# Kernel optimization log

Measured on AMD Instinct MI355X. Metric: run time of the kernel, lower is better.

The kernel has to match this reference:

```python
import jax, jax.numpy as jnp
import numpy as np

B, S, D = 8, 4096, 512
EPS = 1e-6


def setup_inputs() -> dict:
    key = jax.random.key(0)
    ks = jax.random.split(key, 9)
    scale = 1.0 / np.sqrt(D)
    inp = {
        "x_seq": jax.random.normal(ks[0], (B, S, D), dtype=jnp.float32),
        "Wq": jax.random.uniform(ks[1], (D, D), jnp.float32, -scale, scale),
        "bq": jax.random.uniform(ks[2], (D,), jnp.float32, -scale, scale),
        "Wk": jax.random.uniform(ks[3], (D, D), jnp.float32, -scale, scale),
        "bk": jax.random.uniform(ks[4], (D,), jnp.float32, -scale, scale),
        "Wv": jax.random.uniform(ks[5], (D, D), jnp.float32, -scale, scale),
        "bv": jax.random.uniform(ks[6], (D,), jnp.float32, -scale, scale),
        "Wa": jax.random.uniform(ks[7], (D, D), jnp.float32, -scale, scale),
        "ba": jax.random.uniform(ks[8], (D,), jnp.float32, -scale, scale),
    }
    return inp


def _forward(x_seq, Wq, bq, Wk, bk, Wv, bv, Wa, ba):
    # Precompute all projections for the whole sequence (big GEMMs).
    q = jax.nn.relu(jnp.einsum('bsd,ed->bse', x_seq, Wq) + bq)  # phi = relu
    k = jax.nn.relu(jnp.einsum('bsd,ed->bse', x_seq, Wk) + bk)
    v = jnp.einsum('bsd,ed->bse', x_seq, Wv) + bv
    a = jax.nn.sigmoid(jnp.einsum('bsd,ed->bse', x_seq, Wa) + ba)

    # time-major for scan: (S, B, D)
    qs, ks_, vs, as_ = (jnp.swapaxes(t, 0, 1) for t in (q, k, v, a))

    def step(carry, inp):
        s, z = carry                      # s: (B,D,D), z: (B,D)
        q_t, k_t, v_t, a_t = inp
        s = a_t[:, :, None] * s + k_t[:, :, None] * v_t[:, None, :]
        z = a_t * z + k_t
        num = jnp.einsum('bi,bij->bj', q_t, s)
        den = jnp.sum(q_t * z, axis=-1, keepdims=True) + EPS
        return (s, z), num / den

    s0 = jnp.zeros((x_seq.shape[0], x_seq.shape[2], x_seq.shape[2]), x_seq.dtype)
    z0 = jnp.zeros((x_seq.shape[0], x_seq.shape[2]), x_seq.dtype)
    _, ys = jax.lax.scan(step, (s0, z0), (qs, ks_, vs, as_))
    return jnp.swapaxes(ys, 0, 1)  # (B, S, D)


def reference(x_seq, Wq, bq, Wk, bk, Wv, bv, Wa, ba):
    return _forward(x_seq, Wq, bq, Wk, bk, Wv, bv, Wa, ba)
```

## Files before the change

kernel.cpp:

```cpp
#include <hip/hip_runtime.h>
#include <hip/hip_bf16.h>
#include <cstdint>
#include <cstddef>

#define D_DIM 512
#define B_DIM 8
#define S_DIM 4096
#define M_DIM (B_DIM * S_DIM)
#define CHUNK 64
#define NCHUNK (S_DIM / CHUNK)
#define NSEG 8
#define CSEG (NCHUNK / NSEG)
#define EPS_C 1e-6f

typedef __attribute__((ext_vector_type(8))) short bf16x8;
typedef __attribute__((ext_vector_type(4))) float f32x4;

#define GLOAD_LDS16(src, dst)                                              \
  __builtin_amdgcn_global_load_lds(                                        \
      (const __attribute__((address_space(1))) void*)(src),                \
      (__attribute__((address_space(3))) void*)(dst), 16, 0, 0)

__device__ __forceinline__ unsigned short f2bf(float f) {
  uint32_t u = __float_as_uint(f);
  u = (u + 0x7fffu + ((u >> 16) & 1u)) >> 16;
  return (unsigned short)u;
}
__device__ __forceinline__ float bf2f(unsigned short s) { return __uint_as_float(((uint32_t)s) << 16); }

__global__ void cvt_f32_bf16(const float* __restrict__ in, unsigned short* __restrict__ out, int n4) {
  int i = blockIdx.x * blockDim.x + threadIdx.x;
  int stride = gridDim.x * blockDim.x;
  for (; i < n4; i += stride) {
    float4 f = ((const float4*)in)[i];
    ushort4 o;
    o.x = f2bf(f.x); o.y = f2bf(f.y); o.z = f2bf(f.z); o.w = f2bf(f.w);
    ((ushort4*)out)[i] = o;
  }
}

#define TM 128
#define TN 128
#define BK 32

__global__ __launch_bounds__(256) void proj_gemm(
    const unsigned short* __restrict__ Xb,
    const unsigned short* __restrict__ Wb,
    const float* __restrict__ bq, const float* __restrict__ bk,
    const float* __restrict__ bv, const float* __restrict__ ba,
    unsigned short* __restrict__ q_ws, unsigned short* __restrict__ k_ws,
    unsigned short* __restrict__ v_ws, unsigned short* __restrict__ g_ws) {
  __shared__ unsigned short SB[TM * BK + TN * BK];
  unsigned short* As = SB;
  unsigned short* Bs = SB + TM * BK;

  const int proj = blockIdx.z;
  const unsigned short* W = Wb + (size_t)proj * D_DIM * D_DIM;
  const int m0 = blockIdx.x * TM;
  const int n0 = blockIdx.y * TN;
  const int tid = threadIdx.x;
  const int lane = tid & 63;
  const int wave = tid >> 6;
  const int wm = (wave & 1) * 64;
  const int wn = (wave >> 1) * 64;
  const int quad = lane >> 4;
  const int l16 = lane & 15;

  f32x4 acc[4][4];
#pragma unroll
  for (int i = 0; i < 4; ++i)
#pragma unroll
    for (int j = 0; j < 4; ++j) acc[i][j] = (f32x4){0.f, 0.f, 0.f, 0.f};

  const int rw = lane >> 2;
  const int kq = (lane & 3) * 8;

  for (int kc = 0; kc < D_DIM; kc += BK) {
    __syncthreads();
    {
      const unsigned short* gA0 = &Xb[(size_t)(m0 + wave * 16 + rw) * D_DIM + kc + kq];
      const unsigned short* gA1 = &Xb[(size_t)(m0 + 64 + wave * 16 + rw) * D_DIM + kc + kq];
      const unsigned short* gB0 = &W[(size_t)(n0 + wave * 16 + rw) * D_DIM + kc + kq];
      const unsigned short* gB1 = &W[(size_t)(n0 + 64 + wave * 16 + rw) * D_DIM + kc + kq];
      GLOAD_LDS16(gA0, &As[(wave * 16) * BK]);
      GLOAD_LDS16(gA1, &As[(64 + wave * 16) * BK]);
      GLOAD_LDS16(gB0, &Bs[(wave * 16) * BK]);
      GLOAD_LDS16(gB1, &Bs[(64 + wave * 16) * BK]);
    }
    __syncthreads();

    bf16x8 afr[4], bfr[4];
#pragma unroll
    for (int im = 0; im < 4; ++im)
      afr[im] = *(const bf16x8*)&As[(wm + im * 16 + l16) * BK + quad * 8];
#pragma unroll
    for (int in = 0; in < 4; ++in)
      bfr[in] = *(const bf16x8*)&Bs[(wn + in * 16 + l16) * BK + quad * 8];
#pragma unroll
    for (int im = 0; im < 4; ++im)
#pragma unroll
      for (int in = 0; in < 4; ++in)
        acc[im][in] = __builtin_amdgcn_mfma_f32_16x16x32_bf16(afr[im], bfr[in], acc[im][in], 0, 0, 0);
  }

  __syncthreads();

  const float* bias = (proj == 0) ? bq : (proj == 1) ? bk : (proj == 2) ? bv : ba;
  unsigned short* outp = (proj == 0) ? q_ws : (proj == 1) ? k_ws : (proj == 2) ? v_ws : g_ws;
  const bool do_relu = (proj <= 1);
  unsigned short* EP = &SB[wave * 64 * 32];

#pragma unroll
  for (int p = 0; p < 2; ++p) {
#pragma unroll
    for (int half = 0; half < 2; ++half) {
      const int in = 2 * p + half;
      const int nn = n0 + wn + in * 16 + l16;
      const float bn = bias[nn];
#pragma unroll
      for (int im = 0; im < 4; ++im) {
#pragma unroll
        for (int vv = 0; vv < 4; ++vv) {
          float val = acc[im][in][vv] + bn;
          if (do_relu) val = fmaxf(val, 0.f);
          EP[(im * 16 + quad * 4 + vv) * 32 + half * 16 + l16] = f2bf(val);
        }
      }
    }
#pragma unroll
    for (int it = 0; it < 4; ++it) {
      const int row = it * 16 + (lane >> 2);
      const int ccol = (lane & 3) * 8;
      bf16x8 vdat = *(const bf16x8*)&EP[row * 32 + ccol];
      size_t gidx = (size_t)(m0 + wm + row) * D_DIM + (size_t)(n0 + wn + p * 32 + ccol);
      *(bf16x8*)&outp[gidx] = vdat;
    }
  }
}

__global__ __launch_bounds__(512) void prep(
    const unsigned short* __restrict__ q, const unsigned short* __restrict__ k,
    const unsigned short* __restrict__ g,
    unsigned short* __restrict__ qt, unsigned short* __restrict__ kt,
    unsigned short* __restrict__ kh,
    float* __restrict__ Af, float* __restrict__ khs) {
  __shared__ float segp[8][512];
  const int c = blockIdx.x, b = blockIdx.y;
  const int seg = threadIdx.x >> 6;
  const int t = threadIdx.x & 63;
  const int i0 = t * 8;
  const int r0 = seg * 8;
  const size_t t0 = (size_t)b * S_DIM + (size_t)c * CHUNK;
  const size_t cb = ((size_t)b * NCHUNK + c) * D_DIM;

  float sp[8];
#pragma unroll
  for (int j = 0; j < 8; ++j) sp[j] = 1.f;
  for (int r = 0; r < 8; ++r) {
    bf16x8 gv = *(const bf16x8*)&g[(t0 + r0 + r) * D_DIM + i0];
#pragma unroll
    for (int j = 0; j < 8; ++j)
      sp[j] *= 1.f / (1.f + __expf(-bf2f((unsigned short)gv[j])));
  }
  *(float4*)&segp[seg][i0] = *(float4*)&sp[0];
  *(float4*)&segp[seg][i0 + 4] = *(float4*)&sp[4];
  __syncthreads();

  float pre[8], tot[8];
#pragma unroll
  for (int j = 0; j < 8; ++j) { pre[j] = 1.f; tot[j] = 1.f; }
  for (int s2 = 0; s2 < 8; ++s2) {
    float4 v0 = *(const float4*)&segp[s2][i0];
    float4 v1 = *(const float4*)&segp[s2][i0 + 4];
    float v[8] = {v0.x, v0.y, v0.z, v0.w, v1.x, v1.y, v1.z, v1.w};
#pragma unroll
    for (int j = 0; j < 8; ++j) {
      tot[j] *= v[j];
      if (s2 < seg) pre[j] *= v[j];
    }
  }
  if (seg == 0) {
    float4 a0 = {tot[0], tot[1], tot[2], tot[3]};
    float4 a1 = {tot[4], tot[5], tot[6], tot[7]};
    *(float4*)&Af[cb + i0] = a0;
    *(float4*)&Af[cb + i0 + 4] = a1;
  }

  float cum[8], ssum[8];
#pragma unroll
  for (int j = 0; j < 8; ++j) { cum[j] = pre[j]; ssum[j] = 0.f; }
  for (int r = 0; r < 8; ++r) {
    size_t idx = (t0 + r0 + r) * D_DIM + i0;
    bf16x8 gv = *(const bf16x8*)&g[idx];
    bf16x8 qv8 = *(const bf16x8*)&q[idx];
    bf16x8 kv8 = *(const bf16x8*)&k[idx];
    bf16x8 oq, ok, okh;
#pragma unroll
    for (int j = 0; j < 8; ++j) {
      cum[j] *= 1.f / (1.f + __expf(-bf2f((unsigned short)gv[j])));
      float qv = bf2f((unsigned short)qv8[j]);
      float kv = bf2f((unsigned short)kv8[j]);
      oq[j] = (short)f2bf(qv * cum[j]);
      float inv = 1.f / cum[j];
      ok[j] = (short)f2bf(kv * inv);
      float khf = kv * (tot[j] * inv);
      okh[j] = (short)f2bf(khf);
      ssum[j] += khf;
    }
    *(bf16x8*)&qt[idx] = oq;
    *(bf16x8*)&kt[idx] = ok;
    *(bf16x8*)&kh[idx] = okh;
  }

  __syncthreads();
  *(float4*)&segp[seg][i0] = *(float4*)&ssum[0];
  *(float4*)&segp[seg][i0 + 4] = *(float4*)&ssum[4];
  __syncthreads();
  if (seg == 0) {
    float s[8];
#pragma unroll
    for (int j = 0; j < 8; ++j) s[j] = 0.f;
    for (int s2 = 0; s2 < 8; ++s2) {
      float4 v0 = *(const float4*)&segp[s2][i0];
      float4 v1 = *(const float4*)&segp[s2][i0 + 4];
      s[0] += v0.x; s[1] += v0.y; s[2] += v0.z; s[3] += v0.w;
      s[4] += v1.x; s[5] += v1.y; s[6] += v1.z; s[7] += v1.w;
    }
    float4 a0 = {s[0], s[1], s[2], s[3]};
    float4 a1 = {s[4], s[5], s[6], s[7]};
    *(float4*)&khs[cb + i0] = a0;
    *(float4*)&khs[cb + i0 + 4] = a1;
  }
}

__global__ __launch_bounds__(256) void transpose_cd(
    const unsigned short* __restrict__ in, unsigned short* __restrict__ outT) {
  __shared__ unsigned short tile[CHUNK][264];
  const int c = blockIdx.x, b = blockIdx.y;
  const size_t base_in = ((size_t)b * S_DIM + (size_t)c * CHUNK) * D_DIM;
  const size_t base_out = ((size_t)b * NCHUNK + c) * (size_t)D_DIM * CHUNK;
  const int tid = threadIdx.x;
#pragma unroll
  for (int h = 0; h < 2; ++h) {
    if (h) __syncthreads();
#pragma unroll
    for (int it = 0; it < 8; ++it) {
      int flat = (it * 256 + tid) * 8;
      int row = flat >> 8;
      int col = flat & 255;
      *(uint4*)&tile[row][col] = *(const uint4*)&in[base_in + (size_t)row * D_DIM + h * 256 + col];
    }
    __syncthreads();
#pragma unroll
    for (int it = 0; it < 8; ++it) {
      int wq = it * 256 + tid;
      int i_loc = wq >> 3;
      int r0 = (wq & 7) * 8;
      ushort4 v0, v1;
      v0.x = tile[r0 + 0][i_loc]; v0.y = tile[r0 + 1][i_loc];
      v0.z = tile[r0 + 2][i_loc]; v0.w = tile[r0 + 3][i_loc];
      v1.x = tile[r0 + 4][i_loc]; v1.y = tile[r0 + 5][i_loc];
      v1.z = tile[r0 + 6][i_loc]; v1.w = tile[r0 + 7][i_loc];
      size_t o = base_out + (size_t)(h * 256 + i_loc) * CHUNK + r0;
      *(ushort4*)&outT[o] = v0;
      *(ushort4*)&outT[o + 4] = v1;
    }
  }
}

__global__ __launch_bounds__(256) void intra(
    const unsigned short* __restrict__ qt, const unsigned short* kt,
    const unsigned short* __restrict__ VT,
    unsigned short* numI, float* __restrict__ rs) {
  __shared__ unsigned short P_lds[CHUNK][CHUNK + 8];
  const int c = blockIdx.x, b = blockIdx.y;
  const size_t t0 = (size_t)b * S_DIM + (size_t)c * CHUNK;
  const int lane = threadIdx.x & 63, w = threadIdx.x >> 6;
  const int l16 = lane & 15, q4 = lane >> 4;

  f32x4 accP[4];
#pragma unroll
  for (int n = 0; n < 4; ++n) accP[n] = (f32x4){0.f, 0.f, 0.f, 0.f};
#pragma unroll
  for (int ks = 0; ks < 16; ++ks) {
    bf16x8 afr = *(const bf16x8*)&qt[(t0 + 16 * w + l16) * D_DIM + 32 * ks + 8 * q4];
#pragma unroll
    for (int n = 0; n < 4; ++n) {
      bf16x8 bfr = *(const bf16x8*)&kt[(t0 + 16 * n + l16) * D_DIM + 32 * ks + 8 * q4];
      accP[n] = __builtin_amdgcn_mfma_f32_16x16x32_bf16(afr, bfr, accP[n], 0, 0, 0);
    }
  }
  float rsum[4] = {0.f, 0.f, 0.f, 0.f};
#pragma unroll
  for (int n = 0; n < 4; ++n) {
    int m = 16 * n + l16;
#pragma unroll
    for (int vv = 0; vv < 4; ++vv) {
      int r = 16 * w + 4 * q4 + vv;
      float pv = (m <= r) ? accP[n][vv] : 0.f;
      rsum[vv] += pv;
      P_lds[r][m] = f2bf(pv);
    }
  }
#pragma unroll
  for (int msk = 1; msk < 16; msk <<= 1) {
#pragma unroll
    for (int vv = 0; vv < 4; ++vv) rsum[vv] += __shfl_xor(rsum[vv], msk, 64);
  }
  if (l16 == 0) {
#pragma unroll
    for (int vv = 0; vv < 4; ++vv) rs[t0 + 16 * w + 4 * q4 + vv] = rsum[vv];
  }
  __syncthreads();
  bf16x8 pa0 = *(const bf16x8*)&P_lds[16 * w + l16][8 * q4];
  bf16x8 pa1 = *(const bf16x8*)&P_lds[16 * w + l16][32 + 8 * q4];
  const size_t vtb = ((size_t)b * NCHUNK + c) * (size_t)D_DIM * CHUNK;
#pragma unroll 4
  for (int nt = 0; nt < 32; ++nt) {
    bf16x8 b0 = *(const bf16x8*)&VT[vtb + (size_t)(nt * 16 + l16) * CHUNK + 8 * q4];
    bf16x8 b1 = *(const bf16x8*)&VT[vtb + (size_t)(nt * 16 + l16) * CHUNK + 32 + 8 * q4];
    f32x4 acc = (f32x4){0.f, 0.f, 0.f, 0.f};
    acc = __builtin_amdgcn_mfma_f32_16x16x32_bf16(pa0, b0, acc, 0, 0, 0);
    acc = __builtin_amdgcn_mfma_f32_16x16x32_bf16(pa1, b1, acc, 0, 0, 0);
#pragma unroll
    for (int vv = 0; vv < 4; ++vv)
      numI[(t0 + 16 * w + 4 * q4 + vv) * D_DIM + nt * 16 + l16] = f2bf(acc[vv]);
  }
}

__global__ __launch_bounds__(512) void zscan(
    const float* __restrict__ Af, const float* __restrict__ khs,
    float* __restrict__ zall, float* __restrict__ Pseg) {
  const int b = blockIdx.x;
  const int i = threadIdx.x;
  float z = 0.f, rp = 1.f;
  for (int c = 0; c < NCHUNK; ++c) {
    const size_t cb = ((size_t)b * NCHUNK + c) * D_DIM;
    zall[cb + i] = z;
    float af = Af[cb + i];
    z = fmaf(af, z, khs[cb + i]);
    rp *= af;
    if ((c & (CSEG - 1)) == CSEG - 1) {
      Pseg[((size_t)b * NSEG + (c / CSEG)) * D_DIM + i] = rp;
      rp = 1.f;
    }
  }
}

__global__ __launch_bounds__(512) void denk(
    const unsigned short* __restrict__ qt, const float* __restrict__ zall,
    float* rs_invden) {
  const int c = blockIdx.x, b = blockIdx.y;
  const int lane = threadIdx.x & 63, w = threadIdx.x >> 6;
  const size_t t0 = (size_t)b * S_DIM + (size_t)c * CHUNK;
  const size_t zb = ((size_t)b * NCHUNK + c) * D_DIM;
  float4 z0 = *(const float4*)&zall[zb + lane * 8];
  float4 z1 = *(const float4*)&zall[zb + lane * 8 + 4];
#pragma unroll
  for (int rr = 0; rr < 8; ++rr) {
    int r = 8 * w + rr;
    bf16x8 qv = *(const bf16x8*)&qt[(t0 + r) * D_DIM + lane * 8];
    float p = 0.f;
    p = fmaf(bf2f((unsigned short)qv[0]), z0.x, p);
    p = fmaf(bf2f((unsigned short)qv[1]), z0.y, p);
    p = fmaf(bf2f((unsigned short)qv[2]), z0.z, p);
    p = fmaf(bf2f((unsigned short)qv[3]), z0.w, p);
    p = fmaf(bf2f((unsigned short)qv[4]), z1.x, p);
    p = fmaf(bf2f((unsigned short)qv[5]), z1.y, p);
    p = fmaf(bf2f((unsigned short)qv[6]), z1.z, p);
    p = fmaf(bf2f((unsigned short)qv[7]), z1.w, p);
#pragma unroll
    for (int msk = 1; msk < 64; msk <<= 1) p += __shfl_xor(p, msk, 64);
    if (lane == 0) {
      float* iv = &rs_invden[t0 + r];
      *iv = 1.f / (p + *iv + EPS_C);
    }
  }
}

__global__ __launch_bounds__(512, 2) void useg_k(
    const unsigned short* __restrict__ khT, const unsigned short* __restrict__ VT,
    const float* __restrict__ Af, unsigned short* __restrict__ U) {
  __shared__ unsigned short VTl[2][128 * 64];
  const int s = blockIdx.x, jt = blockIdx.y, b = blockIdx.z;
  const int lane = threadIdx.x & 63, w = threadIdx.x >> 6;
  const int l16 = lane & 15, q4 = lane >> 4;
  const int j0 = jt * 128;
  const int iw = 64 * w;
  const int vrow = lane >> 3;
  const int vswz = (lane & 7) ^ (vrow & 7);

  f32x4 acc[4][8];
#pragma unroll
  for (int T = 0; T < 4; ++T)
#pragma unroll
    for (int h = 0; h < 8; ++h) acc[T][h] = (f32x4){0.f, 0.f, 0.f, 0.f};

  const size_t cb0 = ((size_t)b * NCHUNK + s * CSEG) * D_DIM;
  {
    const size_t ob0 = cb0 * CHUNK;
#pragma unroll
    for (int kk = 0; kk < 2; ++kk) {
      const int k = 2 * w + kk;
      GLOAD_LDS16(&VT[ob0 + (size_t)(j0 + 8 * k + vrow) * CHUNK + vswz * 8],
                  &VTl[0][k * 512]);
    }
  }
  bf16x8 a0[4], a1[4];
  {
    const size_t ob0 = cb0 * CHUNK;
#pragma unroll
    for (int T = 0; T < 4; ++T) {
      a0[T] = *(const bf16x8*)&khT[ob0 + (size_t)(iw + 16 * T + l16) * CHUNK + 8 * q4];
      a1[T] = *(const bf16x8*)&khT[ob0 + (size_t)(iw + 16 * T + l16) * CHUNK + 32 + 8 * q4];
    }
  }

  for (int cc = 0; cc < CSEG; ++cc) {
    const size_t cb = cb0 + (size_t)cc * D_DIM;
    __syncthreads();
    if (cc + 1 < CSEG) {
      const size_t obn = (cb + D_DIM) * CHUNK;
#pragma unroll
      for (int kk = 0; kk < 2; ++kk) {
        const int k = 2 * w + kk;
        GLOAD_LDS16(&VT[obn + (size_t)(j0 + 8 * k + vrow) * CHUNK + vswz * 8],
                    &VTl[(cc + 1) & 1][k * 512]);
      }
    }
#pragma unroll
    for (int T = 0; T < 4; ++T) {
      float4 af = *(const float4*)&Af[cb + iw + 16 * T + 4 * q4];
#pragma unroll
      for (int h = 0; h < 8; ++h) {
        acc[T][h][0] *= af.x; acc[T][h][1] *= af.y; acc[T][h][2] *= af.z; acc[T][h][3] *= af.w;
      }
    }
    const unsigned short* Vb = VTl[cc & 1];
#pragma unroll
    for (int h = 0; h < 8; ++h) {
      const int jpos = 16 * h + l16;
      const int swz = jpos & 7;
      bf16x8 bv0 = *(const bf16x8*)&Vb[jpos * 64 + ((q4 ^ swz) * 8)];
      bf16x8 bv1 = *(const bf16x8*)&Vb[jpos * 64 + (((4 + q4) ^ swz) * 8)];
#pragma unroll
      for (int T = 0; T < 4; ++T) {
        acc[T][h] = __builtin_amdgcn_mfma_f32_16x16x32_bf16(a0[T], bv0, acc[T][h], 0, 0, 0);
        acc[T][h] = __builtin_amdgcn_mfma_f32_16x16x32_bf16(a1[T], bv1, acc[T][h], 0, 0, 0);
      }
    }
    if (cc + 1 < CSEG) {
      const size_t obn = (cb + D_DIM) * CHUNK;
#pragma unroll
      for (int T = 0; T < 4; ++T) {
        a0[T] = *(const bf16x8*)&khT[obn + (size_t)(iw + 16 * T + l16) * CHUNK + 8 * q4];
        a1[T] = *(const bf16x8*)&khT[obn + (size_t)(iw + 16 * T + l16) * CHUNK + 32 + 8 * q4];
      }
    }
  }
  const size_t ub = ((size_t)b * NSEG + s) * D_DIM;
#pragma unroll
  for (int T = 0; T < 4; ++T)
#pragma unroll
    for (int h = 0; h < 8; ++h) {
      uint2 pk;
      pk.x = (uint32_t)f2bf(acc[T][h][0]) | ((uint32_t)f2bf(acc[T][h][1]) << 16);
      pk.y = (uint32_t)f2bf(acc[T][h][2]) | ((uint32_t)f2bf(acc[T][h][3]) << 16);
      *(uint2*)&U[(ub + j0 + 16 * h + l16) * (size_t)D_DIM + iw + 16 * T + 4 * q4] = pk;
    }
}

__global__ __launch_bounds__(256) void sscan(
    const float* __restrict__ Pseg, unsigned short* __restrict__ U) {
  const int b = blockIdx.y;
  const int flat = blockIdx.x * 256 + threadIdx.x;
  const int j = flat >> 6;
  const int i0 = (flat & 63) * 8;
  float acc[8];
#pragma unroll
  for (int t = 0; t < 8; ++t) acc[t] = 0.f;
  for (int s = 0; s < NSEG; ++s) {
    const size_t pb = ((size_t)b * NSEG + s) * D_DIM;
    unsigned short* up = &U[(pb + j) * (size_t)D_DIM + i0];
    uint4 u = *(const uint4*)up;
    float4 p0 = *(const float4*)&Pseg[pb + i0];
    float4 p1 = *(const float4*)&Pseg[pb + i0 + 4];
    float uv[8];
    uv[0] = bf2f((unsigned short)(u.x & 0xffff)); uv[1] = bf2f((unsigned short)(u.x >> 16));
    uv[2] = bf2f((unsigned short)(u.y & 0xffff)); uv[3] = bf2f((unsigned short)(u.y >> 16));
    uv[4] = bf2f((unsigned short)(u.z & 0xffff)); uv[5] = bf2f((unsigned short)(u.z >> 16));
    uv[6] = bf2f((unsigned short)(u.w & 0xffff)); uv[7] = bf2f((unsigned short)(u.w >> 16));
    uint4 o;
    o.x = (uint32_t)f2bf(acc[0]) | ((uint32_t)f2bf(acc[1]) << 16);
    o.y = (uint32_t)f2bf(acc[2]) | ((uint32_t)f2bf(acc[3]) << 16);
    o.z = (uint32_t)f2bf(acc[4]) | ((uint32_t)f2bf(acc[5]) << 16);
    o.w = (uint32_t)f2bf(acc[6]) | ((uint32_t)f2bf(acc[7]) << 16);
    *(uint4*)up = o;
    acc[0] = fmaf(p0.x, acc[0], uv[0]);
    acc[1] = fmaf(p0.y, acc[1], uv[1]);
    acc[2] = fmaf(p0.z, acc[2], uv[2]);
    acc[3] = fmaf(p0.w, acc[3], uv[3]);
    acc[4] = fmaf(p1.x, acc[4], uv[4]);
    acc[5] = fmaf(p1.y, acc[5], uv[5]);
    acc[6] = fmaf(p1.z, acc[6], uv[6]);
    acc[7] = fmaf(p1.w, acc[7], uv[7]);
  }
}

__global__ __launch_bounds__(512, 2) void scan2(
    const unsigned short* __restrict__ qt, const unsigned short* __restrict__ khT,
    const unsigned short* __restrict__ VT, const float* __restrict__ Af,
    const unsigned short* __restrict__ Sin,
    const unsigned short* __restrict__ numI, const float* __restrict__ invden,
    float* __restrict__ out) {
  __shared__ unsigned short STj[128][520];
  __shared__ unsigned short VTl[128 * 64];
  const int s = blockIdx.x, jt = blockIdx.y, b = blockIdx.z;
  const int lane = threadIdx.x & 63, w = threadIdx.x >> 6;
  const int l16 = lane & 15, q4 = lane >> 4;
  const int j0 = jt * 128;
  const int iw = 64 * w;
  const int rw = 16 * (w & 3);
  const int jo = 64 * (w >> 2);
  const int vrow = lane >> 3;
  const int vswz = (lane & 7) ^ (vrow & 7);

  f32x4 acc[4][8];

  {
    const size_t pb = ((size_t)b * NSEG + s) * D_DIM;
#pragma unroll
    for (int T = 0; T < 4; ++T)
#pragma unroll
      for (int h = 0; h < 8; ++h) {
        uint2 uu = *(const uint2*)&Sin[(pb + j0 + 16 * h + l16) * (size_t)D_DIM + iw + 16 * T + 4 * q4];
        acc[T][h][0] = bf2f((unsigned short)(uu.x & 0xffff));
        acc[T][h][1] = bf2f((unsigned short)(uu.x >> 16));
        acc[T][h][2] = bf2f((unsigned short)(uu.y & 0xffff));
        acc[T][h][3] = bf2f((unsigned short)(uu.y >> 16));
      }
  }

  for (int cc = 0; cc < CSEG; ++cc) {
    const int c = s * CSEG + cc;
    const size_t cb = ((size_t)b * NCHUNK + c) * D_DIM;
    const size_t t0 = (size_t)b * S_DIM + (size_t)c * CHUNK;
    const size_t ob = cb * CHUNK;
    const bool upd = (cc != CSEG - 1);

    bf16x8 a0[4], a1[4];
    if (upd) {
#pragma unroll
      for (int kk = 0; kk < 2; ++kk) {
        const int k = 2 * w + kk;
        GLOAD_LDS16(&VT[ob + (size_t)(j0 + 8 * k + vrow) * CHUNK + vswz * 8],
                    &VTl[k * 512]);
      }
#pragma unroll
      for (int T = 0; T < 4; ++T) {
        a0[T] = *(const bf16x8*)&khT[ob + (size_t)(iw + 16 * T + l16) * CHUNK + 8 * q4];
        a1[T] = *(const bf16x8*)&khT[ob + (size_t)(iw + 16 * T + l16) * CHUNK + 32 + 8 * q4];
      }
    }

#pragma unroll
    for (int T = 0; T < 4; ++T)
#pragma unroll
      for (int h = 0; h < 8; ++h) {
        uint2 pk;
        pk.x = (uint32_t)f2bf(acc[T][h][0]) | ((uint32_t)f2bf(acc[T][h][1]) << 16);
        pk.y = (uint32_t)f2bf(acc[T][h][2]) | ((uint32_t)f2bf(acc[T][h][3]) << 16);
        *(uint2*)&STj[16 * h + l16][iw + 16 * T + 4 * q4] = pk;
      }
    __syncthreads();

    {
      f32x4 accO[4];
#pragma unroll
      for (int h = 0; h < 4; ++h) accO[h] = (f32x4){0.f, 0.f, 0.f, 0.f};
#pragma unroll
      for (int ks = 0; ks < 16; ++ks) {
        bf16x8 afr = *(const bf16x8*)&qt[(t0 + rw + l16) * D_DIM + 32 * ks + 8 * q4];
#pragma unroll
        for (int h = 0; h < 4; ++h) {
          bf16x8 bfr = *(const bf16x8*)&STj[jo + 16 * h + l16][32 * ks + 8 * q4];
          accO[h] = __builtin_amdgcn_mfma_f32_16x16x32_bf16(afr, bfr, accO[h], 0, 0, 0);
        }
      }
#pragma unroll
      for (int h = 0; h < 4; ++h)
#pragma unroll
        for (int vv = 0; vv < 4; ++vv) {
          size_t t = t0 + rw + 4 * q4 + vv;
          int j = j0 + jo + 16 * h + l16;
          float idv = invden[t];
          float nI = bf2f(numI[t * D_DIM + j]);
          out[t * D_DIM + j] = (accO[h][vv] + nI) * idv;
        }
    }

    if (upd) {
#pragma unroll
      for (int T = 0; T < 4; ++T) {
        float4 af = *(const float4*)&Af[cb + iw + 16 * T + 4 * q4];
#pragma unroll
        for (int h = 0; h < 8; ++h) {
          acc[T][h][0] *= af.x; acc[T][h][1] *= af.y; acc[T][h][2] *= af.z; acc[T][h][3] *= af.w;
        }
      }
#pragma unroll
      for (int h = 0; h < 8; ++h) {
        const int jpos = 16 * h + l16;
        const int swz = jpos & 7;
        bf16x8 bv0 = *(const bf16x8*)&VTl[jpos * 64 + ((q4 ^ swz) * 8)];
        bf16x8 bv1 = *(const bf16x8*)&VTl[jpos * 64 + (((4 + q4) ^ swz) * 8)];
#pragma unroll
        for (int T = 0; T < 4; ++T) {
          acc[T][h] = __builtin_amdgcn_mfma_f32_16x16x32_bf16(a0[T], bv0, acc[T][h], 0, 0, 0);
          acc[T][h] = __builtin_amdgcn_mfma_f32_16x16x32_bf16(a1[T], bv1, acc[T][h], 0, 0, 0);
        }
      }
    }
    __syncthreads();
  }
}

extern "C" void kernel_launch(void* const* d_in, const int* in_sizes, int n_in,
                              void* d_out, int out_size, void* d_ws, size_t ws_size,
                              hipStream_t stream) {
  const float* x  = (const float*)d_in[0];
  const float* Wq = (const float*)d_in[1];
  const float* bq = (const float*)d_in[2];
  const float* Wk = (const float*)d_in[3];
  const float* bk = (const float*)d_in[4];
  const float* Wv = (const float*)d_in[5];
  const float* bv = (const float*)d_in[6];
  const float* Wa = (const float*)d_in[7];
  const float* ba = (const float*)d_in[8];
  float* out = (float*)d_out;

  const size_t MD2 = (size_t)M_DIM * D_DIM * 2;
  uint8_t* w = (uint8_t*)d_ws;
  unsigned short* xb   = (unsigned short*)w; w += MD2;
  unsigned short* wb   = (unsigned short*)w; w += (size_t)4 * D_DIM * D_DIM * 2;
  unsigned short* q_ws = (unsigned short*)w; w += MD2;
  unsigned short* k_ws = (unsigned short*)w; w += MD2;
  unsigned short* v_ws = (unsigned short*)w; w += MD2;
  unsigned short* g_ws = (unsigned short*)w; w += MD2;
  float* Af     = (float*)w; w += (size_t)B_DIM * NCHUNK * D_DIM * 4;
  float* khs    = (float*)w; w += (size_t)B_DIM * NCHUNK * D_DIM * 4;
  float* invden = (float*)w; w += (size_t)M_DIM * 4;

  unsigned short* qt   = xb;
  unsigned short* kt   = q_ws;
  unsigned short* kh   = k_ws;
  unsigned short* VT   = g_ws;
  unsigned short* khT  = v_ws;
  unsigned short* numI = q_ws;
  unsigned short* U    = k_ws;
  float* zall = (float*)wb;
  float* Pseg = (float*)((uint8_t*)wb + (1 << 20));

  cvt_f32_bf16<<<1024, 256, 0, stream>>>(x, xb, M_DIM * D_DIM / 4);
  cvt_f32_bf16<<<128, 256, 0, stream>>>(Wq, wb + 0 * D_DIM * D_DIM, D_DIM * D_DIM / 4);
  cvt_f32_bf16<<<128, 256, 0, stream>>>(Wk, wb + 1 * D_DIM * D_DIM, D_DIM * D_DIM / 4);
  cvt_f32_bf16<<<128, 256, 0, stream>>>(Wv, wb + 2 * D_DIM * D_DIM, D_DIM * D_DIM / 4);
  cvt_f32_bf16<<<128, 256, 0, stream>>>(Wa, wb + 3 * D_DIM * D_DIM, D_DIM * D_DIM / 4);

  proj_gemm<<<dim3(M_DIM / TM, D_DIM / TN, 4), 256, 0, stream>>>(
      xb, wb, bq, bk, bv, ba, q_ws, k_ws, v_ws, g_ws);

  prep<<<dim3(NCHUNK, B_DIM), 512, 0, stream>>>(q_ws, k_ws, g_ws, qt, kt, kh, Af, khs);
  transpose_cd<<<dim3(NCHUNK, B_DIM), 256, 0, stream>>>(v_ws, VT);
  transpose_cd<<<dim3(NCHUNK, B_DIM), 256, 0, stream>>>(kh, khT);
  zscan<<<B_DIM, 512, 0, stream>>>(Af, khs, zall, Pseg);
  intra<<<dim3(NCHUNK, B_DIM), 256, 0, stream>>>(qt, kt, VT, numI, invden);
  denk<<<dim3(NCHUNK, B_DIM), 512, 0, stream>>>(qt, zall, invden);
  useg_k<<<dim3(NSEG, 4, B_DIM), 512, 0, stream>>>(khT, VT, Af, U);
  sscan<<<dim3(128, B_DIM), 256, 0, stream>>>(Pseg, U);
  scan2<<<dim3(NSEG, 4, B_DIM), 512, 0, stream>>>(qt, khT, VT, Af, U, numI, invden, out);
}
```

Measured before the change: 505.8 us.

## Enlarge projection GEMM tiles with double-buffered swizzled LDS staging

Result: no change. 508.3 us (+0.5%).

```diff
diff --git a/kernel.cpp b/kernel.cpp
--- a/kernel.cpp
+++ b/kernel.cpp
@@ -39,96 +39,103 @@
   }
 }
 
-#define TM 128
-#define TN 128
-#define BK 32
-
-__global__ __launch_bounds__(256) void proj_gemm(
+#define PTM 256
+#define PTN 256
+#define PBK 64
+
+__global__ __launch_bounds__(512, 2) void proj_gemm(
     const unsigned short* __restrict__ Xb,
     const unsigned short* __restrict__ Wb,
     const float* __restrict__ bq, const float* __restrict__ bk,
     const float* __restrict__ bv, const float* __restrict__ ba,
     unsigned short* __restrict__ q_ws, unsigned short* __restrict__ k_ws,
     unsigned short* __restrict__ v_ws, unsigned short* __restrict__ g_ws) {
-  __shared__ unsigned short SB[TM * BK + TN * BK];
-  unsigned short* As = SB;
-  unsigned short* Bs = SB + TM * BK;
+  __shared__ unsigned short SB[2 * (PTM + PTN) * PBK];
 
   const int proj = blockIdx.z;
   const unsigned short* W = Wb + (size_t)proj * D_DIM * D_DIM;
-  const int m0 = blockIdx.x * TM;
-  const int n0 = blockIdx.y * TN;
-  const int tid = threadIdx.x;
-  const int lane = tid & 63;
-  const int wave = tid >> 6;
-  const int wm = (wave & 1) * 64;
-  const int wn = (wave >> 1) * 64;
-  const int quad = lane >> 4;
-  const int l16 = lane & 15;
-
-  f32x4 acc[4][4];
-#pragma unroll
-  for (int i = 0; i < 4; ++i)
-#pragma unroll
-    for (int j = 0; j < 4; ++j) acc[i][j] = (f32x4){0.f, 0.f, 0.f, 0.f};
-
-  const int rw = lane >> 2;
-  const int kq = (lane & 3) * 8;
-
-  for (int kc = 0; kc < D_DIM; kc += BK) {
+  const int m0 = blockIdx.x * PTM;
+  const int n0 = blockIdx.y * PTN;
+  const int lane = threadIdx.x & 63;
+  const int w = threadIdx.x >> 6;
+  const int l16 = lane & 15, q4 = lane >> 4;
+  const int wm = (w >> 2) * 128;
+  const int wn = (w & 3) * 64;
+
+  f32x4 acc[8][4];
+#pragma unroll
+  for (int m = 0; m < 8; ++m)
+#pragma unroll
+    for (int n = 0; n < 4; ++n) acc[m][n] = (f32x4){0.f, 0.f, 0.f, 0.f};
+
+  const int srow = lane >> 3;
+  const int sg = lane & 7;
+
+  auto STAGE = [&](int buf, int kc) {
+    unsigned short* A = SB + buf * ((PTM + PTN) * PBK);
+    unsigned short* Bs = A + PTM * PBK;
+#pragma unroll
+    for (int q = 0; q < 4; ++q) {
+      const int row = w * 32 + q * 8 + srow;
+      const int g = sg ^ (row & 7);
+      GLOAD_LDS16(&Xb[(size_t)(m0 + row) * D_DIM + kc + g * 8], &A[(w * 32 + q * 8) * PBK]);
+      GLOAD_LDS16(&W[(size_t)(n0 + row) * D_DIM + kc + g * 8], &Bs[(w * 32 + q * 8) * PBK]);
+    }
+  };
+
+  STAGE(0, 0);
+  __syncthreads();
+
+  for (int t = 0; t < D_DIM / PBK; ++t) {
+    const int cur = t & 1;
+    if (t + 1 < D_DIM / PBK) STAGE(cur ^ 1, (t + 1) * PBK);
+
+    const unsigned short* A = SB + cur * ((PTM + PTN) * PBK);
+    const unsigned short* Bs = A + PTM * PBK;
+    const int rsw = l16 & 7;
+#pragma unroll
+    for (int ks = 0; ks < 2; ++ks) {
+      const int gphys = ((ks * 4 + q4) ^ rsw) * 8;
+      bf16x8 afr[8], bfr[4];
+#pragma unroll
+      for (int m = 0; m < 8; ++m)
+        afr[m] = *(const bf16x8*)&A[(wm + m * 16 + l16) * PBK + gphys];
+#pragma unroll
+      for (int n = 0; n < 4; ++n)
+        bfr[n] = *(const bf16x8*)&Bs[(wn + n * 16 + l16) * PBK + gphys];
+#pragma unroll
+      for (int m = 0; m < 8; ++m)
+#pragma unroll
+        for (int n = 0; n < 4; ++n)
+          acc[m][n] = __builtin_amdgcn_mfma_f32_16x16x32_bf16(afr[m], bfr[n], acc[m][n], 0, 0, 0);
+    }
     __syncthreads();
-    {
-      const unsigned short* gA0 = &Xb[(size_t)(m0 + wave * 16 + rw) * D_DIM + kc + kq];
-      const unsigned short* gA1 = &Xb[(size_t)(m0 + 64 + wave * 16 + rw) * D_DIM + kc + kq];
-      const unsigned short* gB0 = &W[(size_t)(n0 + wave * 16 + rw) * D_DIM + kc + kq];
-      const unsigned short* gB1 = &W[(size_t)(n0 + 64 + wave * 16 + rw) * D_DIM + kc + kq];
-      GLOAD_LDS16(gA0, &As[(wave * 16) * BK]);
-      GLOAD_LDS16(gA1, &As[(64 + wave * 16) * BK]);
-      GLOAD_LDS16(gB0, &Bs[(wave * 16) * BK]);
-      GLOAD_LDS16(gB1, &Bs[(64 + wave * 16) * BK]);
-    }
-    __syncthreads();
-
-    bf16x8 afr[4], bfr[4];
-#pragma unroll
-    for (int im = 0; im < 4; ++im)
-      afr[im] = *(const bf16x8*)&As[(wm + im * 16 + l16) * BK + quad * 8];
-#pragma unroll
-    for (int in = 0; in < 4; ++in)
-      bfr[in] = *(const bf16x8*)&Bs[(wn + in * 16 + l16) * BK + quad * 8];
-#pragma unroll
-    for (int im = 0; im < 4; ++im)
-#pragma unroll
-      for (int in = 0; in < 4; ++in)
-        acc[im][in] = __builtin_amdgcn_mfma_f32_16x16x32_bf16(afr[im], bfr[in], acc[im][in], 0, 0, 0);
-  }
-
-  __syncthreads();
+  }
 
   const float* bias = (proj == 0) ? bq : (proj == 1) ? bk : (proj == 2) ? bv : ba;
   unsigned short* outp = (proj == 0) ? q_ws : (proj == 1) ? k_ws : (proj == 2) ? v_ws : g_ws;
   const bool do_relu = (proj <= 1);
-  unsigned short* EP = &SB[wave * 64 * 32];
+  unsigned short* EP = &SB[w * 128 * 32];
 
 #pragma unroll
   for (int p = 0; p < 2; ++p) {
 #pragma unroll
     for (int half = 0; half < 2; ++half) {
-      const int in = 2 * p + half;
-      const int nn = n0 + wn + in * 16 + l16;
+      const int in_idx = p * 2 + half;
+      const int nn = n0 + wn + in_idx * 16 + l16;
       const float bn = bias[nn];
 #pragma unroll
-      for (int im = 0; im < 4; ++im) {
+      for (int m = 0; m < 8; ++m) {
 #pragma unroll
         for (int vv = 0; vv < 4; ++vv) {
-          float val = acc[im][in][vv] + bn;
+          float val = acc[m][in_idx][vv] + bn;
           if (do_relu) val = fmaxf(val, 0.f);
-          EP[(im * 16 + quad * 4 + vv) * 32 + half * 16 + l16] = f2bf(val);
+          EP[(m * 16 + q4 * 4 + vv) * 32 + half * 16 + l16] = f2bf(val);
         }
       }
     }
 #pragma unroll
-    for (int it = 0; it < 4; ++it) {
+    for (int it = 0; it < 8; ++it) {
       const int row = it * 16 + (lane >> 2);
       const int ccol = (lane & 3) * 8;
       bf16x8 vdat = *(const bf16x8*)&EP[row * 32 + ccol];
@@ -667,7 +674,7 @@
   cvt_f32_bf16<<<128, 256, 0, stream>>>(Wv, wb + 2 * D_DIM * D_DIM, D_DIM * D_DIM / 4);
   cvt_f32_bf16<<<128, 256, 0, stream>>>(Wa, wb + 3 * D_DIM * D_DIM, D_DIM * D_DIM / 4);
 
-  proj_gemm<<<dim3(M_DIM / TM, D_DIM / TN, 4), 256, 0, stream>>>(
+  proj_gemm<<<dim3(M_DIM / PTM, D_DIM / PTN, 4), 512, 0, stream>>>(
       xb, wb, bq, bk, bv, ba, q_ws, k_ws, v_ws, g_ws);
 
   prep<<<dim3(NCHUNK, B_DIM), 512, 0, stream>>>(q_ws, k_ws, g_ws, qt, kt, kh, Af, khs);
```
